# Performance work log

Hardware: AMD Instinct MI355X
Metric: run time of the kernel (lower is better)

The kernel has to match this reference:

```python
import jax, jax.numpy as jnp
import numpy as np

N_NODES = 100000
N_EDGES = 1600000
HIDDEN = 128
N_ETYPES = 4
N_STEPS = 4


def setup_inputs() -> dict:
    key = jax.random.key(0)
    ks = jax.random.split(key, 10)
    s = 1.0 / np.sqrt(HIDDEN)
    node_feat = jax.random.normal(ks[0], (N_NODES, HIDDEN), dtype=jnp.float32)
    edge_index = jax.random.randint(ks[1], (2, N_EDGES), 0, N_NODES)
    edge_feat = jax.random.uniform(ks[2], (N_EDGES, N_ETYPES), dtype=jnp.float32)
    # per-edge-type linear layers (DGL GatedGraphConv uses nn.Linear per etype)
    W_edge = jax.random.uniform(ks[3], (N_ETYPES, HIDDEN, HIDDEN), minval=-s, maxval=s, dtype=jnp.float32)
    b_edge = jax.random.uniform(ks[4], (N_ETYPES, HIDDEN), minval=-s, maxval=s, dtype=jnp.float32)
    # GRUCell parameters (torch layout: gates stacked r, z, n)
    W_ih = jax.random.uniform(ks[5], (3 * HIDDEN, HIDDEN), minval=-s, maxval=s, dtype=jnp.float32)
    W_hh = jax.random.uniform(ks[6], (3 * HIDDEN, HIDDEN), minval=-s, maxval=s, dtype=jnp.float32)
    b_ih = jax.random.uniform(ks[7], (3 * HIDDEN,), minval=-s, maxval=s, dtype=jnp.float32)
    b_hh = jax.random.uniform(ks[8], (3 * HIDDEN,), minval=-s, maxval=s, dtype=jnp.float32)
    return {"node_feat": node_feat, "edge_index": edge_index, "edge_feat": edge_feat,
            "W_edge": W_edge, "b_edge": b_edge, "W_ih": W_ih, "W_hh": W_hh,
            "b_ih": b_ih, "b_hh": b_hh}


def _gru_cell(x, h, W_ih, W_hh, b_ih, b_hh):
    gi = x @ W_ih.T + b_ih  # (N, 3D)
    gh = h @ W_hh.T + b_hh
    ir, iz, inn = jnp.split(gi, 3, axis=1)
    hr, hz, hn = jnp.split(gh, 3, axis=1)
    r = jax.nn.sigmoid(ir + hr)
    z = jax.nn.sigmoid(iz + hz)
    n = jnp.tanh(inn + r * hn)
    return (1.0 - z) * n + z * h


def reference(node_feat, edge_index, edge_feat, W_edge, b_edge, W_ih, W_hh, b_ih, b_hh):
    etypes = jnp.argmax(edge_feat, axis=1)          # (E,)
    src, dst = edge_index[0], edge_index[1]
    N = node_feat.shape[0]
    h = node_feat
    for _ in range(N_STEPS):
        # per-etype linear transform of all nodes: (T, N, D)
        trans = jnp.einsum('nd,tod->tno', h, W_edge) + b_edge[:, None, :]
        msg = trans[etypes, src]                    # (E, D) gather by (etype, src)
        a = jax.ops.segment_sum(msg, dst, num_segments=N)  # scatter-add to dst
        h = _gru_cell(a, h, W_ih, W_hh, b_ih, b_hh)
    return h
```

## Files before the change

### kernel.cpp

```cpp
#include <hip/hip_runtime.h>

#define N_NODES 100000
#define N_EDGES 1600000
#define HID 128
#define SCAN_N (N_NODES*4)
#define NB1 ((SCAN_N + 1023) / 1024)
#define ZERO_IDX (N_NODES*4)

#define EB 8192
#define NBLKA ((N_EDGES + EB - 1) / EB)
#define BSH 9
#define NBUCK ((N_NODES + (1<<BSH) - 1) >> BSH)
#define N2 (NBUCK * NBLKA)
#define NB2 ((N2 + 1023) / 1024)

typedef __attribute__((ext_vector_type(8))) short short8;
typedef __attribute__((ext_vector_type(4))) float float4v;
typedef __attribute__((ext_vector_type(4))) int int4v;
typedef __attribute__((ext_vector_type(2))) unsigned int uint2v;
typedef unsigned short ushort_t;
typedef unsigned int uint_t;

__device__ __forceinline__ float bits2f(uint_t u){ union{uint_t u; float f;} x; x.u=u; return x.f; }
__device__ __forceinline__ float b2f(ushort_t u){ return bits2f(((uint_t)u)<<16); }
__device__ __forceinline__ ushort_t f2b(float f){
  union{float f; uint_t u;} x; x.f=f;
  uint_t r = x.u + 0x7fffu + ((x.u>>16)&1u);
  return (ushort_t)(r>>16);
}
__device__ __forceinline__ float sigm(float x){ return 1.0f/(1.0f+__expf(-x)); }
__device__ __forceinline__ float tanh_f(float x){
  float t=__expf(-2.0f*fabsf(x)); float y=(1.0f-t)/(1.0f+t); return x>=0.f? y : -y;
}
__device__ __forceinline__ int imin(int a, int b){ return a < b ? a : b; }


__global__ void prep_weights(const float* __restrict__ W_edge, const float* __restrict__ W_ih,
                             const float* __restrict__ W_hh, ushort_t* __restrict__ WY,
                             ushort_t* __restrict__ W2f, ushort_t* __restrict__ WYf){
  int i = blockIdx.x*256 + threadIdx.x;
  if (i < 65536){
    WY[i] = f2b(W_edge[i]);
  } else if (i < 65536 + 131072){
    int i2 = i - 65536;
    int tile = i2 >> 9, e9 = i2 & 511;
    int lane = e9 >> 3, e = e9 & 7;
    int kk = tile & 1, kt = (tile >> 1) & 3, j = (tile >> 3) & 7, wn = tile >> 6;
    int lq = lane >> 4, l15 = lane & 15;
    int c = wn*32 + (j&1)*16 + l15;
    int jg = j >> 1;
    int k = kt*64 + (kk*4 + lq)*8 + e;
    float v;
    if (jg < 2)       v = (k < 128) ? W_ih[(jg*128 + c)*128 + k] : W_hh[(jg*128 + c)*128 + (k-128)];
    else if (jg == 2) v = (k < 128) ? W_ih[(256 + c)*128 + k] : 0.0f;
    else              v = (k >= 128) ? W_hh[(256 + c)*128 + (k-128)] : 0.0f;
    W2f[i2] = f2b(v);
  } else if (i < 65536 + 131072 + 65536){
    int i3 = i - 65536 - 131072;
    int tile = i3 >> 9, e9 = i3 & 511;
    int lane = e9 >> 3, e = e9 & 7;
    int kc = tile & 3, j = (tile >> 2) & 3, wn = (tile >> 4) & 3, nh = tile >> 6;
    int lq = lane >> 4, l15 = lane & 15;
    int n = nh*256 + wn*64 + j*16 + l15;
    int k = kc*32 + lq*8 + e;
    WYf[i3] = f2b(W_edge[n*128 + k]);
  }
}

__global__ void edge_pass1(const int* __restrict__ eidx, const float* __restrict__ efeat,
                           int* __restrict__ packed, int* __restrict__ cnt,
                           int* __restrict__ bcntT){
  __shared__ int hist[NBUCK];
  int tid = threadIdx.x, blk = blockIdx.x;
  for (int j = tid; j < NBUCK; j += 512) hist[j] = 0;
  __syncthreads();
  #pragma unroll
  for (int k = 0; k < EB/512; ++k){
    int e = blk*EB + k*512 + tid;
    if (e < N_EDGES){
      int src = eidx[e], dst = eidx[N_EDGES + e];
      float4v f = *(const float4v*)(efeat + (size_t)e*4);
      int t = 0; float b = f[0];
      if (f[1] > b){ b = f[1]; t = 1; }
      if (f[2] > b){ b = f[2]; t = 2; }
      if (f[3] > b){ b = f[3]; t = 3; }
      packed[e] = (src << 2) | t;
      atomicAdd(&cnt[dst*4 + t], 1);
      atomicAdd(&hist[dst >> BSH], 1);
    }
  }
  __syncthreads();
  for (int j = tid; j < NBUCK; j += 512) bcntT[j*NBLKA + blk] = hist[j];
}

__global__ void scan_pass1(const int* __restrict__ src, int* __restrict__ bsum, int n){
  __shared__ int ws[4];
  int tid = threadIdx.x, lane = tid & 63, w = tid >> 6;
  int idx = blockIdx.x*1024 + tid*4;
  int v = 0;
  if (idx + 3 < n){ int4v x = *(const int4v*)(src + idx); v = x[0]+x[1]+x[2]+x[3]; }
  else { for (int k = 0; k < 4; ++k) if (idx + k < n) v += src[idx+k]; }
  for (int d = 32; d; d >>= 1) v += __shfl_down(v, d);
  if (lane == 0) ws[w] = v;
  __syncthreads();
  if (tid == 0) bsum[blockIdx.x] = ws[0]+ws[1]+ws[2]+ws[3];
}

__global__ void scan_pass2(const int* __restrict__ bsum, int* __restrict__ bpre,
                           int* __restrict__ total_out, int nb){
  __shared__ int sh[512];
  int tid = threadIdx.x;
  int v = (tid < nb) ? bsum[tid] : 0;
  sh[tid] = v;
  __syncthreads();
  for (int d = 1; d < 512; d <<= 1){
    int y = (tid >= d) ? sh[tid-d] : 0;
    __syncthreads();
    sh[tid] += y;
    __syncthreads();
  }
  if (tid < nb) bpre[tid] = sh[tid] - v;
  if (tid == 511) *total_out = sh[511];
}

__global__ void scan_pass3(const int* __restrict__ src, const int* __restrict__ bpre,
                           int* __restrict__ off, int n){
  __shared__ int wsum[4];
  int tid = threadIdx.x, lane = tid & 63, w = tid >> 6;
  int idx = blockIdx.x*1024 + tid*4;
  int v0=0,v1=0,v2=0,v3=0;
  if (idx + 3 < n){ int4v x = *(const int4v*)(src + idx); v0=x[0];v1=x[1];v2=x[2];v3=x[3]; }
  else {
    if (idx   < n) v0 = src[idx];
    if (idx+1 < n) v1 = src[idx+1];
    if (idx+2 < n) v2 = src[idx+2];
    if (idx+3 < n) v3 = src[idx+3];
  }
  int ts = v0+v1+v2+v3;
  int sc = ts;
  for (int d = 1; d < 64; d <<= 1){ int y = __shfl_up(sc, d); if (lane >= d) sc += y; }
  if (lane == 63) wsum[w] = sc;
  __syncthreads();
  int wofs = 0;
  for (int k = 0; k < w; ++k) wofs += wsum[k];
  int base = bpre[blockIdx.x] + wofs + sc - ts;
  int e0 = base, e1 = e0+v0, e2 = e1+v1, e3 = e2+v2;
  if (idx   < n) off[idx  ] = e0;
  if (idx+1 < n) off[idx+1] = e1;
  if (idx+2 < n) off[idx+2] = e2;
  if (idx+3 < n) off[idx+3] = e3;
}

__global__ void bucket_scatter(const int* __restrict__ eidx, const int* __restrict__ packed,
                               const int* __restrict__ boffT, int* __restrict__ bucketed){
  __shared__ int cur[NBUCK];
  int tid = threadIdx.x, blk = blockIdx.x;
  for (int j = tid; j < NBUCK; j += 512) cur[j] = boffT[j*NBLKA + blk];
  __syncthreads();
  #pragma unroll
  for (int k = 0; k < EB/512; ++k){
    int e = blk*EB + k*512 + tid;
    if (e < N_EDGES){
      int dst = eidx[N_EDGES + e];
      int pos = atomicAdd(&cur[dst >> BSH], 1);
      bucketed[pos] = ((dst & ((1<<BSH)-1)) << 19) | packed[e];
    }
  }
}

__global__ void bucket_sort(const int* __restrict__ bucketed, const int* __restrict__ boffT,
                            const int* __restrict__ off4, int* __restrict__ sorted){
  __shared__ int cur[(1<<BSH)*4];
  int tid = threadIdx.x, b = blockIdx.x;
  int base = b * ((1<<BSH)*4);
  for (int j = tid; j < (1<<BSH)*4; j += 512)
    cur[j] = off4[imin(base + j, SCAN_N)];
  __syncthreads();
  int s = boffT[b*NBLKA];
  int e = boffT[(b+1)*NBLKA];
  for (int i = s + tid; i < e; i += 512){
    int w = bucketed[i];
    int ci = ((w >> 19) << 2) | (w & 3);
    int pos = atomicAdd(&cur[ci], 1);
    sorted[pos] = w & 0x7FFFF;
  }
}

__global__ void init_h(const float* __restrict__ nf, ushort_t* __restrict__ hB, int n4){
  int i = blockIdx.x*256 + threadIdx.x;
  if (i >= n4) return;
  float4v v = *(const float4v*)(nf + (size_t)i*4);
  uint2v u;
  u[0] = (uint_t)f2b(v[0]) | ((uint_t)f2b(v[1])<<16);
  u[1] = (uint_t)f2b(v[2]) | ((uint_t)f2b(v[3])<<16);
  *(uint2v*)(hB + (size_t)i*4) = u;
}


__launch_bounds__(512, 2)
__global__ void transform_kernel(const ushort_t* __restrict__ hB, const ushort_t* __restrict__ WY,
                                 ushort_t* __restrict__ Y){
  __shared__ ushort_t lA[128*64];
  __shared__ ushort_t lB[512*64];
  int tid = threadIdx.x, w = tid >> 6, lane = tid & 63;
  int wm = w >> 2, wn = w & 3;
  int row0 = blockIdx.x * 128;
  float4v acc[4][8] = {};
  for (int kt = 0; kt < 2; ++kt){
    short8 va[2], vb[8];
    #pragma unroll
    for (int i = 0; i < 2; ++i){
      int cidx = i*512 + tid;
      int r = cidx >> 3, ch = cidx & 7;
      int node = row0 + r; if (node >= N_NODES) node = N_NODES-1;
      va[i] = *reinterpret_cast<const short8*>(hB + (size_t)node*128 + kt*64 + ch*8);
    }
    #pragma unroll
    for (int i = 0; i < 8; ++i){
      int cidx = i*512 + tid;
      int n = cidx >> 3, ch = cidx & 7;
      vb[i] = *reinterpret_cast<const short8*>(WY + (size_t)n*128 + kt*64 + ch*8);
    }
    __syncthreads();
    #pragma unroll
    for (int i = 0; i < 2; ++i){
      int cidx = i*512 + tid;
      int r = cidx >> 3, ch = cidx & 7;
      *reinterpret_cast<short8*>(lA + r*64 + ((ch ^ (r&7))<<3)) = va[i];
    }
    #pragma unroll
    for (int i = 0; i < 8; ++i){
      int cidx = i*512 + tid;
      int n = cidx >> 3, ch = cidx & 7;
      *reinterpret_cast<short8*>(lB + n*64 + ((ch ^ (n&7))<<3)) = vb[i];
    }
    __syncthreads();
    #pragma unroll
    for (int kk = 0; kk < 2; ++kk){
      int lch = kk*4 + (lane>>4);
      short8 af[4], bf[8];
      #pragma unroll
      for (int i = 0; i < 4; ++i){
        int r = wm*64 + i*16 + (lane&15);
        af[i] = *reinterpret_cast<const short8*>(lA + r*64 + ((lch ^ (r&7))<<3));
      }
      #pragma unroll
      for (int j = 0; j < 8; ++j){
        int n = wn*128 + j*16 + (lane&15);
        bf[j] = *reinterpret_cast<const short8*>(lB + n*64 + ((lch ^ (n&7))<<3));
      }
      #pragma unroll
      for (int i = 0; i < 4; ++i)
        #pragma unroll
        for (int j = 0; j < 8; ++j)
          acc[i][j] = __builtin_amdgcn_mfma_f32_16x16x32_bf16(af[i], bf[j], acc[i][j], 0, 0, 0);
    }
    __syncthreads();
  }
  #pragma unroll
  for (int i = 0; i < 4; ++i)
    #pragma unroll
    for (int j = 0; j < 8; ++j)
      #pragma unroll
      for (int q = 0; q < 4; ++q){
        int grow = row0 + wm*64 + i*16 + (lane>>4)*4 + q;
        if (grow >= N_NODES) continue;
        int colc = wn*128 + j*16 + (lane&15);
        Y[(size_t)grow*512 + colc] = f2b(acc[i][j][q]);
      }
}

__global__ void agg_kernel(const int* __restrict__ off4, const int* __restrict__ sorted,
                           const ushort_t* __restrict__ Y, const int* __restrict__ cnt,
                           const float* __restrict__ b_edge, ushort_t* __restrict__ aB){
  int wid = (int)((blockIdx.x * blockDim.x + threadIdx.x) >> 6);
  int lane = threadIdx.x & 63;
  if (wid >= N_NODES) return;
  int s = off4[wid*4], e = off4[wid*4+4];
  int col = lane*2;
  float p0=0,p1=0,q0=0,q1=0,r0=0,r1=0,t0=0,t1=0;
  for (int i = s; i < e; i += 16){
    int vv[16];
    #pragma unroll
    for (int k = 0; k < 16; ++k){
      int j = i + k;
      int sv = sorted[imin(j, e-1)];
      vv[k] = __builtin_amdgcn_readfirstlane(j < e ? sv : ZERO_IDX);
    }
    uint_t hv[16];
    #pragma unroll
    for (int k = 0; k < 16; ++k)
      hv[k] = *(const uint_t*)(Y + (size_t)vv[k]*128 + col);
    #pragma unroll
    for (int k = 0; k < 16; ++k){
      float f0 = bits2f((hv[k] & 0xffffu) << 16);
      float f1 = bits2f(hv[k] & 0xffff0000u);
      if ((k&3)==0){ p0+=f0; p1+=f1; }
      else if ((k&3)==1){ q0+=f0; q1+=f1; }
      else if ((k&3)==2){ r0+=f0; r1+=f1; }
      else { t0+=f0; t1+=f1; }
    }
  }
  float s0 = (p0+q0)+(r0+t0);
  float s1 = (p1+q1)+(r1+t1);
  int4v c4 = *(const int4v*)(cnt + wid*4);
  #pragma unroll
  for (int t = 0; t < 4; ++t){
    float cf = (float)c4[t];
    s0 += cf * b_edge[t*128 + col];
    s1 += cf * b_edge[t*128 + col + 1];
  }
  *(uint_t*)(aB + (size_t)wid*128 + col) = (uint_t)f2b(s0) | ((uint_t)f2b(s1) << 16);
}

__launch_bounds__(512, 2)
__global__ void gru_tr_kernel(const ushort_t* __restrict__ aB, ushort_t* __restrict__ hB,
                              const ushort_t* __restrict__ W2f, const ushort_t* __restrict__ WYf,
                              const float* __restrict__ b_ih, const float* __restrict__ b_hh,
                              float* __restrict__ hF, ushort_t* __restrict__ Y, int last){
  __shared__ ushort_t lA[2][8192];
  __shared__ ushort_t lH[16384];
  int tid = threadIdx.x, w = tid >> 6, lane = tid & 63;
  int wm = w >> 2, wn = w & 3;
  int l15 = lane & 15, lq = lane >> 4;
  int row0 = blockIdx.x * 128;

  int cidx0 = tid, r0l = cidx0 >> 3, ch0 = cidx0 & 7;
  int cidx1 = 512 + tid, r1l = cidx1 >> 3, ch1 = cidx1 & 7;
  int node0 = imin(row0 + r0l, N_NODES-1);
  int node1 = imin(row0 + r1l, N_NODES-1);
  size_t aoff0 = (size_t)node0*128 + ch0*8;
  size_t aoff1 = (size_t)node1*128 + ch1*8;
  int wo0 = r0l*64 + ((ch0 ^ (r0l&7))<<3);
  int wo1 = r1l*64 + ((ch1 ^ (r1l&7))<<3);

  {
    short8 va0 = *reinterpret_cast<const short8*>(aB + aoff0);
    short8 va1 = *reinterpret_cast<const short8*>(aB + aoff1);
    *reinterpret_cast<short8*>(&lA[0][wo0]) = va0;
    *reinterpret_cast<short8*>(&lA[0][wo1]) = va1;
  }
  __syncthreads();

  float4v acc[4][8] = {};
  #pragma unroll
  for (int kt = 0; kt < 4; ++kt){
    short8 vn0, vn1;
    if (kt < 3){
      const ushort_t* srcN = (kt+1 < 2) ? aB : hB;
      int koff = ((kt+1)&1)*64;
      vn0 = *reinterpret_cast<const short8*>(srcN + aoff0 + koff);
      vn1 = *reinterpret_cast<const short8*>(srcN + aoff1 + koff);
    }
    bool lo = (kt < 2);
    const ushort_t* lcur = lA[kt&1];
    #pragma unroll
    for (int kk = 0; kk < 2; ++kk){
      int lch = kk*4 + lq;
      short8 af[4];
      #pragma unroll
      for (int i = 0; i < 4; ++i){
        int r = wm*64 + i*16 + l15;
        af[i] = *reinterpret_cast<const short8*>(lcur + r*64 + ((lch ^ (r&7))<<3));
      }
      #pragma unroll
      for (int j = 0; j < 8; ++j){
        if (lo ? (j >= 6) : (j == 4 || j == 5)) continue;
        int tile = ((wn*8 + j)*4 + kt)*2 + kk;
        short8 bf = *reinterpret_cast<const short8*>(W2f + (size_t)tile*512 + lane*8);
        #pragma unroll
        for (int i = 0; i < 4; ++i)
          acc[i][j] = __builtin_amdgcn_mfma_f32_16x16x32_bf16(af[i], bf, acc[i][j], 0, 0, 0);
      }
    }
    if (kt < 3){
      *reinterpret_cast<short8*>(&lA[(kt+1)&1][wo0]) = vn0;
      *reinterpret_cast<short8*>(&lA[(kt+1)&1][wo1]) = vn1;
    }
    __syncthreads();
  }
  #pragma unroll
  for (int i = 0; i < 4; ++i){
    #pragma unroll
    for (int jj = 0; jj < 2; ++jj){
      int c = wn*32 + jj*16 + l15;
      float bir = b_ih[c] + b_hh[c];
      float biz = b_ih[128+c] + b_hh[128+c];
      float bni = b_ih[256+c], bnh = b_hh[256+c];
      int cl = c & 63;
      const ushort_t* lh = lA[c >> 6];
      int ch = c >> 3;
      #pragma unroll
      for (int q = 0; q < 4; ++q){
        int row = wm*64 + i*16 + lq*4 + q;
        int grow = row0 + row;
        float rg = sigm(acc[i][0+jj][q] + bir);
        float zg = sigm(acc[i][2+jj][q] + biz);
        float hn = acc[i][6+jj][q] + bnh;
        float nn = tanh_f(acc[i][4+jj][q] + bni + rg*hn);
        float h = b2f(lh[row*64 + (((cl>>3) ^ (row&7))<<3) + (cl&7)]);
        float out = (1.0f - zg)*nn + zg*h;
        ushort_t ob = f2b(out);
        lH[row*128 + ((ch ^ (row&15))<<3) + (c&7)] = ob;
        if (grow < N_NODES){
          hB[(size_t)grow*128 + c] = ob;
          if (last) hF[(size_t)grow*128 + c] = out;
        }
      }
    }
  }
  if (last) return;
  __syncthreads();
  #pragma unroll
  for (int nh = 0; nh < 2; ++nh){
    float4v acc2[4][4] = {};
    #pragma unroll
    for (int kc = 0; kc < 4; ++kc){
      int lchh = kc*4 + lq;
      short8 af[4];
      #pragma unroll
      for (int i = 0; i < 4; ++i){
        int r = wm*64 + i*16 + l15;
        af[i] = *reinterpret_cast<const short8*>(lH + r*128 + ((lchh ^ (r&15))<<3));
      }
      #pragma unroll
      for (int j = 0; j < 4; ++j){
        int tile = ((nh*4 + wn)*4 + j)*4 + kc;
        short8 bf = *reinterpret_cast<const short8*>(WYf + (size_t)tile*512 + lane*8);
        #pragma unroll
        for (int i = 0; i < 4; ++i)
          acc2[i][j] = __builtin_amdgcn_mfma_f32_16x16x32_bf16(af[i], bf, acc2[i][j], 0, 0, 0);
      }
    }
    #pragma unroll
    for (int i = 0; i < 4; ++i)
      #pragma unroll
      for (int q = 0; q < 4; ++q){
        int grow = row0 + wm*64 + i*16 + lq*4 + q;
        if (grow >= N_NODES) continue;
        #pragma unroll
        for (int j = 0; j < 4; ++j)
          Y[(size_t)grow*512 + nh*256 + wn*64 + j*16 + l15] = f2b(acc2[i][j][q]);
      }
  }
}


extern "C" void kernel_launch(void* const* d_in, const int* in_sizes, int n_in,
                              void* d_out, int out_size, void* d_ws, size_t ws_size,
                              hipStream_t stream) {
  const float* node_feat = (const float*)d_in[0];
  const int*   edge_idx  = (const int*)d_in[1];
  const float* edge_feat = (const float*)d_in[2];
  const float* W_edge    = (const float*)d_in[3];
  const float* b_edge    = (const float*)d_in[4];
  const float* W_ih      = (const float*)d_in[5];
  const float* W_hh      = (const float*)d_in[6];
  const float* b_ih      = (const float*)d_in[7];
  const float* b_hh      = (const float*)d_in[8];
  float* hF = (float*)d_out;

  char* p = (char*)d_ws;
  auto take = [&](size_t bytes) -> char* {
    char* r = p; p += (bytes + 255) & ~(size_t)255; return r;
  };
  ushort_t* WY     = (ushort_t*)take(512*128*2);
  ushort_t* W2f    = (ushort_t*)take(131072*2);
  ushort_t* WYf    = (ushort_t*)take(65536*2);
  int* cnt      = (int*)take((size_t)SCAN_N*4);
  int* off4     = (int*)take((size_t)(SCAN_N+1)*4);
  int* bcntT    = (int*)take((size_t)N2*4);
  int* boffT    = (int*)take((size_t)(N2+1)*4);
  int* bsum     = (int*)take(512*4);
  int* bpre     = (int*)take(512*4);
  int* packed   = (int*)take((size_t)N_EDGES*4);
  int* bucketed = (int*)take((size_t)N_EDGES*4);
  int* sorted   = (int*)take((size_t)N_EDGES*4);
  ushort_t* hB = (ushort_t*)take((size_t)N_NODES*128*2);
  ushort_t* Y  = (ushort_t*)take(((size_t)N_NODES*512 + 256)*2);
  ushort_t* aB = (ushort_t*)take((size_t)N_NODES*128*2);

  hipMemsetAsync(cnt, 0, (size_t)SCAN_N*4, stream);
  hipMemsetAsync(Y + (size_t)N_NODES*512, 0, 256*2, stream);

  prep_weights<<<1024, 256, 0, stream>>>(W_edge, W_ih, W_hh, WY, W2f, WYf);
  edge_pass1<<<NBLKA, 512, 0, stream>>>(edge_idx, edge_feat, packed, cnt, bcntT);
  scan_pass1<<<NB1, 256, 0, stream>>>(cnt, bsum, SCAN_N);
  scan_pass2<<<1, 512, 0, stream>>>(bsum, bpre, off4 + SCAN_N, NB1);
  scan_pass3<<<NB1, 256, 0, stream>>>(cnt, bpre, off4, SCAN_N);
  scan_pass1<<<NB2, 256, 0, stream>>>(bcntT, bsum, N2);
  scan_pass2<<<1, 512, 0, stream>>>(bsum, bpre, boffT + N2, NB2);
  scan_pass3<<<NB2, 256, 0, stream>>>(bcntT, bpre, boffT, N2);
  bucket_scatter<<<NBLKA, 512, 0, stream>>>(edge_idx, packed, boffT, bucketed);
  bucket_sort<<<NBUCK, 512, 0, stream>>>(bucketed, boffT, off4, sorted);
  init_h<<<(N_NODES*32 + 255)/256, 256, 0, stream>>>(node_feat, hB, N_NODES*32);

  int gb = (N_NODES + 127) / 128;
  transform_kernel<<<gb, 512, 0, stream>>>(hB, WY, Y);
  for (int step = 0; step < 4; ++step){
    agg_kernel<<<(N_NODES+3)/4, 256, 0, stream>>>(off4, sorted, Y, cnt, b_edge, aB);
    gru_tr_kernel<<<gb, 512, 0, stream>>>(aB, hB, W2f, WYf, b_ih, b_hh, hF, Y, step == 3);
  }
}
```

Baseline: 815.0 us.

## Shrink GRU tile to 64 rows, raise occupancy, coalesce h stores

The fused GRU and transform kernel now processes 64 node rows per block instead of 128. It halves the shared-memory buffers and accumulator arrays and raises the launch-bounds minimum to 4 blocks per SM, aiming for higher occupancy and more blocks in flight. The per-element scattered stores of h are replaced by vectorized 16-byte writes staged through shared memory. The second GEMM is restructured so each wave covers 128 output columns in one pass, which changes the weight-tile layout in prep_weights. Sigmoid and tanh now use hardware reciprocal approximations, trading a little accuracy for fewer instructions. Weight-fragment reuse per block drops, so more global or L2 weight traffic is likely.

```diff
diff --git a/kernel.cpp b/kernel.cpp
--- a/kernel.cpp
+++ b/kernel.cpp
@@ -28,6 +28,8 @@
   uint_t r = x.u + 0x7fffu + ((x.u>>16)&1u);
   return (ushort_t)(r>>16);
 }
+__device__ __forceinline__ float fsigm(float x){ return __builtin_amdgcn_rcpf(1.0f + __expf(-x)); }
+__device__ __forceinline__ float ftanh(float x){ return 2.0f*__builtin_amdgcn_rcpf(1.0f + __expf(-2.0f*x)) - 1.0f; }
 __device__ __forceinline__ float sigm(float x){ return 1.0f/(1.0f+__expf(-x)); }
 __device__ __forceinline__ float tanh_f(float x){
   float t=__expf(-2.0f*fabsf(x)); float y=(1.0f-t)/(1.0f+t); return x>=0.f? y : -y;
@@ -59,9 +61,9 @@
     int i3 = i - 65536 - 131072;
     int tile = i3 >> 9, e9 = i3 & 511;
     int lane = e9 >> 3, e = e9 & 7;
-    int kc = tile & 3, j = (tile >> 2) & 3, wn = (tile >> 4) & 3, nh = tile >> 6;
+    int kc = tile & 3, j = (tile >> 2) & 7, wn = tile >> 5;
     int lq = lane >> 4, l15 = lane & 15;
-    int n = nh*256 + wn*64 + j*16 + l15;
+    int n = wn*128 + j*16 + l15;
     int k = kc*32 + lq*8 + e;
     WYf[i3] = f2b(W_edge[n*128 + k]);
   }
@@ -313,54 +315,43 @@
   *(uint_t*)(aB + (size_t)wid*128 + col) = (uint_t)f2b(s0) | ((uint_t)f2b(s1) << 16);
 }
 
-__launch_bounds__(512, 2)
+__launch_bounds__(512, 4)
 __global__ void gru_tr_kernel(const ushort_t* __restrict__ aB, ushort_t* __restrict__ hB,
                               const ushort_t* __restrict__ W2f, const ushort_t* __restrict__ WYf,
                               const float* __restrict__ b_ih, const float* __restrict__ b_hh,
                               float* __restrict__ hF, ushort_t* __restrict__ Y, int last){
-  __shared__ ushort_t lA[2][8192];
-  __shared__ ushort_t lH[16384];
+  __shared__ ushort_t lA[2][4096];
+  __shared__ ushort_t lH[8192];
   int tid = threadIdx.x, w = tid >> 6, lane = tid & 63;
   int wm = w >> 2, wn = w & 3;
   int l15 = lane & 15, lq = lane >> 4;
-  int row0 = blockIdx.x * 128;
-
-  int cidx0 = tid, r0l = cidx0 >> 3, ch0 = cidx0 & 7;
-  int cidx1 = 512 + tid, r1l = cidx1 >> 3, ch1 = cidx1 & 7;
-  int node0 = imin(row0 + r0l, N_NODES-1);
-  int node1 = imin(row0 + r1l, N_NODES-1);
-  size_t aoff0 = (size_t)node0*128 + ch0*8;
-  size_t aoff1 = (size_t)node1*128 + ch1*8;
-  int wo0 = r0l*64 + ((ch0 ^ (r0l&7))<<3);
-  int wo1 = r1l*64 + ((ch1 ^ (r1l&7))<<3);
-
-  {
-    short8 va0 = *reinterpret_cast<const short8*>(aB + aoff0);
-    short8 va1 = *reinterpret_cast<const short8*>(aB + aoff1);
-    *reinterpret_cast<short8*>(&lA[0][wo0]) = va0;
-    *reinterpret_cast<short8*>(&lA[0][wo1]) = va1;
-  }
-  __syncthreads();
-
-  float4v acc[4][8] = {};
+  int row0 = blockIdx.x * 64;
+
+  int rS = tid >> 3, chS = tid & 7;
+  int nodeS = imin(row0 + rS, N_NODES-1);
+  size_t aoffS = (size_t)nodeS*128 + chS*8;
+  int woS = rS*64 + ((chS ^ (rS&7))<<3);
+
+  *reinterpret_cast<short8*>(&lA[0][woS]) = *reinterpret_cast<const short8*>(aB + aoffS);
+  __syncthreads();
+
+  float4v acc[2][8] = {};
   #pragma unroll
   for (int kt = 0; kt < 4; ++kt){
-    short8 vn0, vn1;
+    short8 vn = {};
     if (kt < 3){
       const ushort_t* srcN = (kt+1 < 2) ? aB : hB;
-      int koff = ((kt+1)&1)*64;
-      vn0 = *reinterpret_cast<const short8*>(srcN + aoff0 + koff);
-      vn1 = *reinterpret_cast<const short8*>(srcN + aoff1 + koff);
+      vn = *reinterpret_cast<const short8*>(srcN + aoffS + ((kt+1)&1)*64);
     }
     bool lo = (kt < 2);
     const ushort_t* lcur = lA[kt&1];
     #pragma unroll
     for (int kk = 0; kk < 2; ++kk){
       int lch = kk*4 + lq;
-      short8 af[4];
-      #pragma unroll
-      for (int i = 0; i < 4; ++i){
-        int r = wm*64 + i*16 + l15;
+      short8 af[2];
+      #pragma unroll
+      for (int i = 0; i < 2; ++i){
+        int r = wm*32 + i*16 + l15;
         af[i] = *reinterpret_cast<const short8*>(lcur + r*64 + ((lch ^ (r&7))<<3));
       }
       #pragma unroll
@@ -369,18 +360,16 @@
         int tile = ((wn*8 + j)*4 + kt)*2 + kk;
         short8 bf = *reinterpret_cast<const short8*>(W2f + (size_t)tile*512 + lane*8);
         #pragma unroll
-        for (int i = 0; i < 4; ++i)
+        for (int i = 0; i < 2; ++i)
           acc[i][j] = __builtin_amdgcn_mfma_f32_16x16x32_bf16(af[i], bf, acc[i][j], 0, 0, 0);
       }
     }
-    if (kt < 3){
-      *reinterpret_cast<short8*>(&lA[(kt+1)&1][wo0]) = vn0;
-      *reinterpret_cast<short8*>(&lA[(kt+1)&1][wo1]) = vn1;
-    }
+    if (kt < 3)
+      *reinterpret_cast<short8*>(&lA[(kt+1)&1][woS]) = vn;
     __syncthreads();
   }
   #pragma unroll
-  for (int i = 0; i < 4; ++i){
+  for (int i = 0; i < 2; ++i){
     #pragma unroll
     for (int jj = 0; jj < 2; ++jj){
       int c = wn*32 + jj*16 + l15;
@@ -392,57 +381,67 @@
       int ch = c >> 3;
       #pragma unroll
       for (int q = 0; q < 4; ++q){
-        int row = wm*64 + i*16 + lq*4 + q;
-        int grow = row0 + row;
-        float rg = sigm(acc[i][0+jj][q] + bir);
-        float zg = sigm(acc[i][2+jj][q] + biz);
+        int row = wm*32 + i*16 + lq*4 + q;
+        float rg = fsigm(acc[i][0+jj][q] + bir);
+        float zg = fsigm(acc[i][2+jj][q] + biz);
         float hn = acc[i][6+jj][q] + bnh;
-        float nn = tanh_f(acc[i][4+jj][q] + bni + rg*hn);
+        float nn = ftanh(acc[i][4+jj][q] + bni + rg*hn);
         float h = b2f(lh[row*64 + (((cl>>3) ^ (row&7))<<3) + (cl&7)]);
         float out = (1.0f - zg)*nn + zg*h;
-        ushort_t ob = f2b(out);
-        lH[row*128 + ((ch ^ (row&15))<<3) + (c&7)] = ob;
-        if (grow < N_NODES){
-          hB[(size_t)grow*128 + c] = ob;
-          if (last) hF[(size_t)grow*128 + c] = out;
-        }
+        lH[row*128 + ((ch ^ (row&15))<<3) + (c&7)] = f2b(out);
+      }
+    }
+  }
+  __syncthreads();
+  #pragma unroll
+  for (int p = 0; p < 2; ++p){
+    int u = p*512 + tid;
+    int row = u >> 4, uc = u & 15;
+    int grow = row0 + row;
+    if (grow < N_NODES){
+      short8 v = *reinterpret_cast<const short8*>(lH + row*128 + ((uc ^ (row&15))<<3));
+      *reinterpret_cast<short8*>(hB + (size_t)grow*128 + uc*8) = v;
+      if (last){
+        float4v f0, f1;
+        #pragma unroll
+        for (int k = 0; k < 4; ++k) f0[k] = b2f((ushort_t)v[k]);
+        #pragma unroll
+        for (int k = 0; k < 4; ++k) f1[k] = b2f((ushort_t)v[4+k]);
+        *reinterpret_cast<float4v*>(hF + (size_t)grow*128 + uc*8)     = f0;
+        *reinterpret_cast<float4v*>(hF + (size_t)grow*128 + uc*8 + 4) = f1;
       }
     }
   }
   if (last) return;
-  __syncthreads();
-  #pragma unroll
-  for (int nh = 0; nh < 2; ++nh){
-    float4v acc2[4][4] = {};
-    #pragma unroll
-    for (int kc = 0; kc < 4; ++kc){
-      int lchh = kc*4 + lq;
-      short8 af[4];
-      #pragma unroll
-      for (int i = 0; i < 4; ++i){
-        int r = wm*64 + i*16 + l15;
-        af[i] = *reinterpret_cast<const short8*>(lH + r*128 + ((lchh ^ (r&15))<<3));
-      }
-      #pragma unroll
-      for (int j = 0; j < 4; ++j){
-        int tile = ((nh*4 + wn)*4 + j)*4 + kc;
-        short8 bf = *reinterpret_cast<const short8*>(WYf + (size_t)tile*512 + lane*8);
-        #pragma unroll
-        for (int i = 0; i < 4; ++i)
-          acc2[i][j] = __builtin_amdgcn_mfma_f32_16x16x32_bf16(af[i], bf, acc2[i][j], 0, 0, 0);
-      }
-    }
-    #pragma unroll
-    for (int i = 0; i < 4; ++i)
-      #pragma unroll
-      for (int q = 0; q < 4; ++q){
-        int grow = row0 + wm*64 + i*16 + lq*4 + q;
-        if (grow >= N_NODES) continue;
-        #pragma unroll
-        for (int j = 0; j < 4; ++j)
-          Y[(size_t)grow*512 + nh*256 + wn*64 + j*16 + l15] = f2b(acc2[i][j][q]);
-      }
-  }
+  float4v acc2[2][8] = {};
+  #pragma unroll
+  for (int kc = 0; kc < 4; ++kc){
+    int lchh = kc*4 + lq;
+    short8 af[2];
+    #pragma unroll
+    for (int i = 0; i < 2; ++i){
+      int r = wm*32 + i*16 + l15;
+      af[i] = *reinterpret_cast<const short8*>(lH + r*128 + ((lchh ^ (r&15))<<3));
+    }
+    #pragma unroll
+    for (int j = 0; j < 8; ++j){
+      int tile = (wn*8 + j)*4 + kc;
+      short8 bf = *reinterpret_cast<const short8*>(WYf + (size_t)tile*512 + lane*8);
+      #pragma unroll
+      for (int i = 0; i < 2; ++i)
+        acc2[i][j] = __builtin_amdgcn_mfma_f32_16x16x32_bf16(af[i], bf, acc2[i][j], 0, 0, 0);
+    }
+  }
+  #pragma unroll
+  for (int i = 0; i < 2; ++i)
+    #pragma unroll
+    for (int q = 0; q < 4; ++q){
+      int grow = row0 + wm*32 + i*16 + lq*4 + q;
+      if (grow >= N_NODES) continue;
+      #pragma unroll
+      for (int j = 0; j < 8; ++j)
+        Y[(size_t)grow*512 + wn*128 + j*16 + l15] = f2b(acc2[i][q == 0 ? j : j][q]);
+    }
 }
 
 
@@ -496,9 +495,10 @@
   init_h<<<(N_NODES*32 + 255)/256, 256, 0, stream>>>(node_feat, hB, N_NODES*32);
 
   int gb = (N_NODES + 127) / 128;
+  int gb2 = (N_NODES + 63) / 64;
   transform_kernel<<<gb, 512, 0, stream>>>(hB, WY, Y);
   for (int step = 0; step < 4; ++step){
     agg_kernel<<<(N_NODES+3)/4, 256, 0, stream>>>(off4, sorted, Y, cnt, b_edge, aB);
-    gru_tr_kernel<<<gb, 512, 0, stream>>>(aB, hB, W2f, WYf, b_ih, b_hh, hF, Y, step == 3);
-  }
-}
+    gru_tr_kernel<<<gb2, 512, 0, stream>>>(aB, hB, W2f, WYf, b_ih, b_hh, hF, Y, step == 3);
+  }
+}
```

After: 759.0 us. 1.07x faster.
